# Kernel optimization log

Hardware: AMD Instinct MI355X
Metric: run time of the kernel (lower is better)

The kernel has to match this reference:

```python
import jax, jax.numpy as jnp
import numpy as np


def setup_inputs() -> dict:
    key = jax.random.key(0)
    ks = jax.random.split(key, 4)
    B, S, D, H, E = 4, 2048, 1024, 4096, 4
    sd = 1.0 / np.sqrt(D)
    sh = 1.0 / np.sqrt(H)
    return {
        "x": jax.random.normal(ks[0], (B, S, D), jnp.float32),
        "Wr": jax.random.normal(ks[1], (D, E), jnp.float32) * sd,
        "W1": jax.random.normal(ks[2], (E, D, H), jnp.float32) * sd,
        "b1": jnp.zeros((E, H), jnp.float32),
        "W2": jax.random.normal(ks[3], (E, H, D), jnp.float32) * sh,
        "b2": jnp.zeros((E, D), jnp.float32),
        "top_k": 2,
    }


def reference(x, Wr, W1, b1, W2, b2, top_k):
    # Router: softmax over experts, then top-k + renormalize (as in torch code)
    logits = jnp.einsum("bsd,de->bse", x, Wr)              # [B,S,E]
    probs = jax.nn.softmax(logits, axis=-1)
    wk, idx = jax.lax.top_k(probs, top_k)                  # [B,S,K]
    wk = wk / jnp.sum(wk, axis=-1, keepdims=True)
    # Scatter top-k weights back to dense per-expert weights [B,S,E]
    E = probs.shape[-1]
    onehot = jax.nn.one_hot(idx, E, dtype=x.dtype)         # [B,S,K,E]
    weights = jnp.einsum("bsk,bske->bse", wk, onehot)      # [B,S,E]
    # Expert MLPs (Linear-ReLU-Linear), computed dense over experts and
    # combined with the (mostly-zero) routing weights — same math as the
    # gather/scatter loop in the torch module.
    h = jax.nn.relu(jnp.einsum("bsd,edh->bseh", x, W1) + b1)   # [B,S,E,H]
    y = jnp.einsum("bseh,ehd->bsed", h, W2) + b2               # [B,S,E,D]
    out = jnp.einsum("bse,bsed->bsd", weights, y)              # [B,S,D]
    aux_loss = jnp.asarray(0.0, dtype=x.dtype)
    return out, aux_loss
```

## Files before the change

### kernel.cpp

```cpp
#include <hip/hip_runtime.h>
#include <cstdint>
#include <cstddef>

typedef _Float16 f16;
typedef __attribute__((ext_vector_type(8))) f16 f16x8;
typedef __attribute__((ext_vector_type(4))) f16 f16x4;
typedef __attribute__((ext_vector_type(4))) float f32x4;

#define M_TOK 8192
#define DDIM 1024
#define HDIM 4096
#define NEXP 4
#define TOTPAD 16896

__device__ __forceinline__ void async_copy16(const void* g, void* s) {
    __builtin_amdgcn_global_load_lds((__attribute__((address_space(1))) void*)g,
                                     (__attribute__((address_space(3))) void*)s,
                                     16, 0, 0);
}

__global__ __launch_bounds__(256) void router_kernel(
    const float* __restrict__ x, const float* __restrict__ Wr,
    float* __restrict__ wts, int* __restrict__ top2) {
    __shared__ float wr_s[DDIM * NEXP];
    for (int i = threadIdx.x; i < DDIM * NEXP; i += 256) wr_s[i] = Wr[i];
    __syncthreads();
    const int wave = threadIdx.x >> 6, lane = threadIdx.x & 63;
    const int t = blockIdx.x * 4 + wave;
    float a0 = 0.f, a1 = 0.f, a2 = 0.f, a3 = 0.f;
    const float* xr = x + (size_t)t * DDIM;
    for (int i = 0; i < DDIM; i += 256) {
        const int d = i + lane * 4;
        const float4 v = *(const float4*)(xr + d);
        const float* w0 = &wr_s[d * 4];
        a0 += v.x * w0[0] + v.y * w0[4] + v.z * w0[8]  + v.w * w0[12];
        a1 += v.x * w0[1] + v.y * w0[5] + v.z * w0[9]  + v.w * w0[13];
        a2 += v.x * w0[2] + v.y * w0[6] + v.z * w0[10] + v.w * w0[14];
        a3 += v.x * w0[3] + v.y * w0[7] + v.z * w0[11] + v.w * w0[15];
    }
    for (int off = 32; off > 0; off >>= 1) {
        a0 += __shfl_xor(a0, off, 64);
        a1 += __shfl_xor(a1, off, 64);
        a2 += __shfl_xor(a2, off, 64);
        a3 += __shfl_xor(a3, off, 64);
    }
    if (lane == 0) {
        float lg[4] = {a0, a1, a2, a3};
        int i1 = 0;
        for (int e = 1; e < 4; ++e) if (lg[e] > lg[i1]) i1 = e;
        int i2 = -1;
        for (int e = 0; e < 4; ++e) {
            if (e == i1) continue;
            if (i2 < 0 || lg[e] > lg[i2]) i2 = e;
        }
        const float w1 = 1.0f / (1.0f + expf(lg[i2] - lg[i1]));
        float w[4] = {0.f, 0.f, 0.f, 0.f};
        w[i1] = w1; w[i2] = 1.0f - w1;
        float* o = wts + (size_t)t * 4;
        o[0] = w[0]; o[1] = w[1]; o[2] = w[2]; o[3] = w[3];
        top2[t] = i1 | (i2 << 8);
    }
}

__global__ __launch_bounds__(256) void count_kernel(
    const int* __restrict__ top2, int* __restrict__ meta) {
    __shared__ int lc[4];
    if (threadIdx.x < 4) lc[threadIdx.x] = 0;
    __syncthreads();
    const int t = blockIdx.x * 256 + threadIdx.x;
    const int p = top2[t];
    atomicAdd(&lc[p & 0xff], 1);
    atomicAdd(&lc[(p >> 8) & 0xff], 1);
    __syncthreads();
    if (threadIdx.x < 4) atomicAdd(&meta[threadIdx.x], lc[threadIdx.x]);
}

__global__ void offsets_kernel(int* __restrict__ meta) {
    if (threadIdx.x == 0) {
        int off = 0;
        for (int e = 0; e < 4; ++e) {
            const int c = meta[e];
            const int cp = (c + 127) & ~127;
            meta[4 + e] = cp;
            meta[8 + e] = off;
            off += cp;
        }
    }
}

__global__ __launch_bounds__(256) void fill_kernel(
    const int* __restrict__ top2, int* __restrict__ meta,
    int* __restrict__ toklist) {
    __shared__ int lc[4], base[4];
    if (threadIdx.x < 4) lc[threadIdx.x] = 0;
    __syncthreads();
    const int t = blockIdx.x * 256 + threadIdx.x;
    const int p = top2[t];
    const int e1 = p & 0xff, e2 = (p >> 8) & 0xff;
    const int r1 = atomicAdd(&lc[e1], 1);
    const int r2 = atomicAdd(&lc[e2], 1);
    __syncthreads();
    if (threadIdx.x < 4) base[threadIdx.x] = atomicAdd(&meta[12 + threadIdx.x], lc[threadIdx.x]);
    __syncthreads();
    toklist[meta[8 + e1] + base[e1] + r1] = t;
    toklist[meta[8 + e2] + base[e2] + r2] = t;
}

__global__ __launch_bounds__(256) void convert_f16_kernel(
    const float* __restrict__ in, f16* __restrict__ out, int n4) {
    const int i = blockIdx.x * 256 + threadIdx.x;
    if (i < n4) {
        const float4 v = ((const float4*)in)[i];
        f16x4 o = {(f16)v.x, (f16)v.y, (f16)v.z, (f16)v.w};
        ((f16x4*)out)[i] = o;
    }
}

__global__ __launch_bounds__(256) void transpose_f16_kernel(
    const float* __restrict__ in0, f16* __restrict__ out0, int R, int C) {
    __shared__ float tile[32][33];
    const float* in = in0 + (size_t)blockIdx.z * R * C;
    f16* out = out0 + (size_t)blockIdx.z * R * C;
    const int c0 = blockIdx.x * 32, r0 = blockIdx.y * 32;
    const int tx = threadIdx.x & 31;
    const int ty = threadIdx.x >> 5;
#pragma unroll
    for (int i = 0; i < 32; i += 8)
        tile[ty + i][tx] = in[(size_t)(r0 + ty + i) * C + c0 + tx];
    __syncthreads();
#pragma unroll
    for (int i = 0; i < 32; i += 8)
        out[(size_t)(c0 + ty + i) * R + r0 + tx] = (f16)tile[tx][ty + i];
}

template <int MODE>
__global__ __launch_bounds__(256) void gemm_kernel(
    const f16* __restrict__ A, const f16* __restrict__ BT,
    int N, int K,
    const float* __restrict__ bias,
    f16* __restrict__ outH, float* __restrict__ outF,
    const float* __restrict__ wts,
    const int* __restrict__ toklist, const int* __restrict__ meta, int e0) {
    __shared__ __align__(16) f16 As[128 * 64];
    __shared__ __align__(16) f16 Bs[128 * 64];
    const int zz = blockIdx.z;
    const int e = e0 + zz;
    const int m0 = blockIdx.y * 128, n0 = blockIdx.x * 128;

    int cnt = M_TOK, off = 0;
    if (meta) {
        cnt = meta[e];
        const int cp = meta[4 + e];
        off = meta[8 + e];
        if (m0 >= cp) return;
    }

    const f16* BTe = BT + (size_t)zz * N * K;
    const float* be = bias + (size_t)zz * N;

    const int tid = threadIdx.x;
    const int wave = tid >> 6, lane = tid & 63;
    const int wm = wave >> 1, wn = wave & 1;
    const int quad = lane >> 4, l16 = lane & 15;

    f32x4 acc[4][4] = {};

    const int lrb = tid >> 3;
    const int gcoff = (((tid & 7) ^ (lrb & 7)) * 8);
    const f16* ga[4];
    const f16* gb[4];
#pragma unroll
    for (int r = 0; r < 4; ++r) {
        const int lr = r * 32 + lrb;
        const int gm = m0 + lr;
        int arow;
        if (MODE == 0) arow = toklist ? toklist[off + gm] : gm;
        else arow = off + gm;
        ga[r] = A + (size_t)arow * K + gcoff;
        gb[r] = BTe + (size_t)(n0 + lr) * K + gcoff;
    }

    const int swl = l16 & 7;
    for (int k0 = 0; k0 < K; k0 += 64) {
#pragma unroll
        for (int r = 0; r < 4; ++r)
            async_copy16(ga[r] + k0, &As[(r * 256 + tid) * 8]);
#pragma unroll
        for (int r = 0; r < 4; ++r)
            async_copy16(gb[r] + k0, &Bs[(r * 256 + tid) * 8]);
        __syncthreads();
#pragma unroll
        for (int kk = 0; kk < 64; kk += 32) {
            const int kc = kk >> 3;
            f16x8 af[4], bf[4];
#pragma unroll
            for (int i = 0; i < 4; ++i)
                af[i] = *(const f16x8*)&As[(size_t)(wm * 64 + i * 16 + l16) * 64 +
                                           (((kc + quad) ^ swl) << 3)];
#pragma unroll
            for (int j = 0; j < 4; ++j)
                bf[j] = *(const f16x8*)&Bs[(size_t)(wn * 64 + j * 16 + l16) * 64 +
                                           (((kc + quad) ^ swl) << 3)];
#pragma unroll
            for (int i = 0; i < 4; ++i)
#pragma unroll
                for (int j = 0; j < 4; ++j)
                    acc[i][j] = __builtin_amdgcn_mfma_f32_16x16x32_f16(af[i], bf[j], acc[i][j], 0, 0, 0);
        }
        __syncthreads();
    }

#pragma unroll
    for (int i = 0; i < 4; ++i) {
        const int mbase = m0 + wm * 64 + i * 16 + quad * 4;
#pragma unroll
        for (int j = 0; j < 4; ++j) {
            const int n = n0 + wn * 64 + j * 16 + l16;
            const float bv = be[n];
#pragma unroll
            for (int r = 0; r < 4; ++r) {
                const int m = mbase + r;
                float v = acc[i][j][r] + bv;
                if (MODE == 0) {
                    v = v > 0.0f ? v : 0.0f;
                    outH[(size_t)(off + m) * N + n] = (f16)v;
                } else {
                    if (m < cnt) {
                        const int t = toklist ? toklist[off + m] : m;
                        const float w = wts[t * 4 + e];
                        atomicAdd(&outF[(size_t)t * N + n], w * v);
                    }
                }
            }
        }
    }
}

extern "C" void kernel_launch(void* const* d_in, const int* in_sizes, int n_in,
                              void* d_out, int out_size, void* d_ws, size_t ws_size,
                              hipStream_t stream) {
    (void)in_sizes; (void)n_in;
    const float* x  = (const float*)d_in[0];
    const float* Wr = (const float*)d_in[1];
    const float* W1 = (const float*)d_in[2];
    const float* b1 = (const float*)d_in[3];
    const float* W2 = (const float*)d_in[4];
    const float* b2 = (const float*)d_in[5];
    float* out = (float*)d_out;

    char* ws = (char*)d_ws;
    float* wts   = (float*)ws;
    int*   meta  = (int*)(ws + (128 << 10));
    int*   top2  = (int*)(ws + (132 << 10));
    int*   tokl  = (int*)(ws + (164 << 10));
    f16*   xb    = (f16*)(ws + (256 << 10));
    const size_t MBs = 1ull << 20;
    const size_t base = (256 << 10) + 16 * MBs;

    const size_t SPARSE_NEED = (256 << 10) + 80 * MBs + (size_t)TOTPAD * HDIM * sizeof(f16);
    const bool sparse = ws_size >= SPARSE_NEED;

    f16 *w1t, *w2t, *h;
    if (sparse) {
        w1t = (f16*)(ws + base);
        w2t = (f16*)(ws + base + 32 * MBs);
        h   = (f16*)(ws + base + 64 * MBs);
    } else {
        w1t = (f16*)(ws + base);
        w2t = (f16*)(ws + base + 8 * MBs);
        h   = (f16*)(ws + base + 16 * MBs);
    }

    hipMemsetAsync(out, 0, (size_t)out_size * sizeof(float), stream);
    router_kernel<<<M_TOK / 4, 256, 0, stream>>>(x, Wr, wts, top2);
    convert_f16_kernel<<<(M_TOK * DDIM / 4) / 256, 256, 0, stream>>>(x, xb, M_TOK * DDIM / 4);

    if (sparse) {
        hipMemsetAsync(meta, 0, 16 * sizeof(int), stream);
        hipMemsetAsync(tokl, 0, (size_t)TOTPAD * sizeof(int), stream);
        count_kernel<<<M_TOK / 256, 256, 0, stream>>>(top2, meta);
        offsets_kernel<<<1, 64, 0, stream>>>(meta);
        fill_kernel<<<M_TOK / 256, 256, 0, stream>>>(top2, meta, tokl);
        transpose_f16_kernel<<<dim3(HDIM / 32, DDIM / 32, NEXP), 256, 0, stream>>>(W1, w1t, DDIM, HDIM);
        transpose_f16_kernel<<<dim3(DDIM / 32, HDIM / 32, NEXP), 256, 0, stream>>>(W2, w2t, HDIM, DDIM);
        gemm_kernel<0><<<dim3(HDIM / 128, M_TOK / 128, NEXP), 256, 0, stream>>>(
            xb, w1t, HDIM, DDIM, b1, h, nullptr, wts, tokl, meta, 0);
        gemm_kernel<1><<<dim3(DDIM / 128, M_TOK / 128, NEXP), 256, 0, stream>>>(
            h, w2t, DDIM, HDIM, b2, nullptr, out, wts, tokl, meta, 0);
    } else {
        for (int e = 0; e < NEXP; ++e) {
            transpose_f16_kernel<<<dim3(HDIM / 32, DDIM / 32, 1), 256, 0, stream>>>(
                W1 + (size_t)e * DDIM * HDIM, w1t, DDIM, HDIM);
            gemm_kernel<0><<<dim3(HDIM / 128, M_TOK / 128, 1), 256, 0, stream>>>(
                xb, w1t, HDIM, DDIM, b1 + (size_t)e * HDIM, h, nullptr, wts, nullptr, nullptr, e);
            transpose_f16_kernel<<<dim3(DDIM / 32, HDIM / 32, 1), 256, 0, stream>>>(
                W2 + (size_t)e * HDIM * DDIM, w2t, HDIM, DDIM);
            gemm_kernel<1><<<dim3(DDIM / 128, M_TOK / 128, 1), 256, 0, stream>>>(
                h, w2t, DDIM, HDIM, b2 + (size_t)e * DDIM, nullptr, out, wts, nullptr, nullptr, e);
        }
    }
}
```

Baseline: 736.9 us.

## Replace atomic scatter in second expert GEMM with slot outputs plus combine kernel

```diff
diff --git a/kernel.cpp b/kernel.cpp
--- a/kernel.cpp
+++ b/kernel.cpp
@@ -21,7 +21,7 @@
 
 __global__ __launch_bounds__(256) void router_kernel(
     const float* __restrict__ x, const float* __restrict__ Wr,
-    float* __restrict__ wts, int* __restrict__ top2) {
+    float* __restrict__ wts, int* __restrict__ top2, float2* __restrict__ wpair) {
     __shared__ float wr_s[DDIM * NEXP];
     for (int i = threadIdx.x; i < DDIM * NEXP; i += 256) wr_s[i] = Wr[i];
     __syncthreads();
@@ -59,6 +59,7 @@
         float* o = wts + (size_t)t * 4;
         o[0] = w[0]; o[1] = w[1]; o[2] = w[2]; o[3] = w[3];
         top2[t] = i1 | (i2 << 8);
+        wpair[t] = make_float2(w1, 1.0f - w1);
     }
 }
 
@@ -90,7 +91,7 @@
 
 __global__ __launch_bounds__(256) void fill_kernel(
     const int* __restrict__ top2, int* __restrict__ meta,
-    int* __restrict__ toklist) {
+    int* __restrict__ toklist, int2* __restrict__ slotmap) {
     __shared__ int lc[4], base[4];
     if (threadIdx.x < 4) lc[threadIdx.x] = 0;
     __syncthreads();
@@ -102,8 +103,11 @@
     __syncthreads();
     if (threadIdx.x < 4) base[threadIdx.x] = atomicAdd(&meta[12 + threadIdx.x], lc[threadIdx.x]);
     __syncthreads();
-    toklist[meta[8 + e1] + base[e1] + r1] = t;
-    toklist[meta[8 + e2] + base[e2] + r2] = t;
+    const int p1 = meta[8 + e1] + base[e1] + r1;
+    const int p2 = meta[8 + e2] + base[e2] + r2;
+    toklist[p1] = t;
+    toklist[p2] = t;
+    slotmap[t] = make_int2(p1, p2);
 }
 
 __global__ __launch_bounds__(256) void convert_f16_kernel(
@@ -145,7 +149,7 @@
     __shared__ __align__(16) f16 Bs[128 * 64];
     const int zz = blockIdx.z;
     const int e = e0 + zz;
-    const int m0 = blockIdx.y * 128, n0 = blockIdx.x * 128;
+    const int m0 = blockIdx.x * 128, n0 = blockIdx.y * 128;
 
     int cnt = M_TOK, off = 0;
     if (meta) {
@@ -225,15 +229,34 @@
                     v = v > 0.0f ? v : 0.0f;
                     outH[(size_t)(off + m) * N + n] = (f16)v;
                 } else {
-                    if (m < cnt) {
-                        const int t = toklist ? toklist[off + m] : m;
-                        const float w = wts[t * 4 + e];
-                        atomicAdd(&outF[(size_t)t * N + n], w * v);
+                    if (outH) {
+                        outH[(size_t)(off + m) * N + n] = (f16)v;
+                    } else if (m < cnt) {
+                        const float w = wts[m * 4 + e];
+                        atomicAdd(&outF[(size_t)m * N + n], w * v);
                     }
                 }
             }
         }
     }
+}
+
+__global__ __launch_bounds__(256) void combine_kernel(
+    const f16* __restrict__ yseg, const int2* __restrict__ slotmap,
+    const float2* __restrict__ wpair, float* __restrict__ out, int aux_idx) {
+    const int t = blockIdx.x;
+    const int2 p = slotmap[t];
+    const float2 w = wpair[t];
+    const int d = threadIdx.x * 4;
+    const f16x4 a = *(const f16x4*)&yseg[(size_t)p.x * DDIM + d];
+    const f16x4 b = *(const f16x4*)&yseg[(size_t)p.y * DDIM + d];
+    float4 o;
+    o.x = w.x * (float)a[0] + w.y * (float)b[0];
+    o.y = w.x * (float)a[1] + w.y * (float)b[1];
+    o.z = w.x * (float)a[2] + w.y * (float)b[2];
+    o.w = w.x * (float)a[3] + w.y * (float)b[3];
+    *(float4*)&out[(size_t)t * DDIM + d] = o;
+    if (t == 0 && threadIdx.x == 0 && aux_idx >= 0) out[aux_idx] = 0.0f;
 }
 
 extern "C" void kernel_launch(void* const* d_in, const int* in_sizes, int n_in,
@@ -249,30 +272,35 @@
     float* out = (float*)d_out;
 
     char* ws = (char*)d_ws;
-    float* wts   = (float*)ws;
-    int*   meta  = (int*)(ws + (128 << 10));
-    int*   top2  = (int*)(ws + (132 << 10));
-    int*   tokl  = (int*)(ws + (164 << 10));
-    f16*   xb    = (f16*)(ws + (256 << 10));
+    float*  wts   = (float*)ws;
+    int*    meta  = (int*)(ws + (128 << 10));
+    int*    top2  = (int*)(ws + (132 << 10));
+    int*    tokl  = (int*)(ws + (164 << 10));
+    float2* wpair = (float2*)(ws + (240 << 10));
+    int2*   slotm = (int2*)(ws + (304 << 10));
+    f16*    xb    = (f16*)(ws + (512 << 10));
     const size_t MBs = 1ull << 20;
-    const size_t base = (256 << 10) + 16 * MBs;
-
-    const size_t SPARSE_NEED = (256 << 10) + 80 * MBs + (size_t)TOTPAD * HDIM * sizeof(f16);
+    const size_t base = (512 << 10) + 16 * MBs;
+
+    const size_t SPARSE_NEED = (512 << 10) + 80 * MBs + (size_t)TOTPAD * HDIM * sizeof(f16);
     const bool sparse = ws_size >= SPARSE_NEED;
 
-    f16 *w1t, *w2t, *h;
+    const int aux_idx = (out_size == M_TOK * DDIM + 1) ? (M_TOK * DDIM) : -1;
+
+    f16 *w1t, *w2t, *h, *yseg;
     if (sparse) {
-        w1t = (f16*)(ws + base);
-        w2t = (f16*)(ws + base + 32 * MBs);
-        h   = (f16*)(ws + base + 64 * MBs);
+        w1t  = (f16*)(ws + base);
+        w2t  = (f16*)(ws + base + 32 * MBs);
+        h    = (f16*)(ws + base + 64 * MBs);
+        yseg = (f16*)(ws + (512 << 10));
     } else {
         w1t = (f16*)(ws + base);
         w2t = (f16*)(ws + base + 8 * MBs);
         h   = (f16*)(ws + base + 16 * MBs);
-    }
-
-    hipMemsetAsync(out, 0, (size_t)out_size * sizeof(float), stream);
-    router_kernel<<<M_TOK / 4, 256, 0, stream>>>(x, Wr, wts, top2);
+        yseg = nullptr;
+    }
+
+    router_kernel<<<M_TOK / 4, 256, 0, stream>>>(x, Wr, wts, top2, wpair);
     convert_f16_kernel<<<(M_TOK * DDIM / 4) / 256, 256, 0, stream>>>(x, xb, M_TOK * DDIM / 4);
 
     if (sparse) {
@@ -280,22 +308,25 @@
         hipMemsetAsync(tokl, 0, (size_t)TOTPAD * sizeof(int), stream);
         count_kernel<<<M_TOK / 256, 256, 0, stream>>>(top2, meta);
         offsets_kernel<<<1, 64, 0, stream>>>(meta);
-        fill_kernel<<<M_TOK / 256, 256, 0, stream>>>(top2, meta, tokl);
+        fill_kernel<<<M_TOK / 256, 256, 0, stream>>>(top2, meta, tokl, slotm);
         transpose_f16_kernel<<<dim3(HDIM / 32, DDIM / 32, NEXP), 256, 0, stream>>>(W1, w1t, DDIM, HDIM);
         transpose_f16_kernel<<<dim3(DDIM / 32, HDIM / 32, NEXP), 256, 0, stream>>>(W2, w2t, HDIM, DDIM);
-        gemm_kernel<0><<<dim3(HDIM / 128, M_TOK / 128, NEXP), 256, 0, stream>>>(
+        gemm_kernel<0><<<dim3(M_TOK / 128, HDIM / 128, NEXP), 256, 0, stream>>>(
             xb, w1t, HDIM, DDIM, b1, h, nullptr, wts, tokl, meta, 0);
-        gemm_kernel<1><<<dim3(DDIM / 128, M_TOK / 128, NEXP), 256, 0, stream>>>(
-            h, w2t, DDIM, HDIM, b2, nullptr, out, wts, tokl, meta, 0);
+        gemm_kernel<1><<<dim3(M_TOK / 128, DDIM / 128, NEXP), 256, 0, stream>>>(
+            h, w2t, DDIM, HDIM, b2, yseg, nullptr, wts, tokl, meta, 0);
+        combine_kernel<<<M_TOK, 256, 0, stream>>>(yseg, slotm, wpair, out, aux_idx);
     } else {
+        hipMemsetAsync(out, 0, (size_t)out_size * sizeof(float), stream);
+        if (aux_idx < 0) {  }
         for (int e = 0; e < NEXP; ++e) {
             transpose_f16_kernel<<<dim3(HDIM / 32, DDIM / 32, 1), 256, 0, stream>>>(
                 W1 + (size_t)e * DDIM * HDIM, w1t, DDIM, HDIM);
-            gemm_kernel<0><<<dim3(HDIM / 128, M_TOK / 128, 1), 256, 0, stream>>>(
+            gemm_kernel<0><<<dim3(M_TOK / 128, HDIM / 128, 1), 256, 0, stream>>>(
                 xb, w1t, HDIM, DDIM, b1 + (size_t)e * HDIM, h, nullptr, wts, nullptr, nullptr, e);
             transpose_f16_kernel<<<dim3(DDIM / 32, HDIM / 32, 1), 256, 0, stream>>>(
                 W2 + (size_t)e * HDIM * DDIM, w2t, HDIM, DDIM);
-            gemm_kernel<1><<<dim3(DDIM / 128, M_TOK / 128, 1), 256, 0, stream>>>(
+            gemm_kernel<1><<<dim3(M_TOK / 128, DDIM / 128, 1), 256, 0, stream>>>(
                 h, w2t, DDIM, HDIM, b2 + (size_t)e * DDIM, nullptr, out, wts, nullptr, nullptr, e);
         }
     }
```

Result: no change. 751.5 us (+2.0%).
